# Kernel optimization log

Measured on AMD Instinct MI355X. Metric: run time of the kernel, lower is better.

## Reference

```python
import jax, jax.numpy as jnp
import numpy as np

B, N, M, C = 4, 4096, 4096, 256
IMG_W, IMG_H = 1242.0, 376.0  # KITTI-like image extents for keypoint coords


def setup_inputs() -> dict:
    key = jax.random.key(0)
    ks = jax.random.split(key, 12)
    s = 1.0 / np.sqrt(C)
    scale_uv = jnp.array([IMG_W, IMG_H], dtype=jnp.float32)
    return {
        "nodes_L": jax.random.normal(ks[0], (B, N, C), jnp.float32),
        "nodes_R": jax.random.normal(ks[1], (B, M, C), jnp.float32),
        "kpts_L": jax.random.uniform(ks[2], (B, N, 2), jnp.float32) * scale_uv,
        "kpts_R": jax.random.uniform(ks[3], (B, M, 2), jnp.float32) * scale_uv,
        "Wq": jax.random.normal(ks[4], (C, C), jnp.float32) * s,
        "bq": jnp.zeros((C,), jnp.float32),
        "Wk": jax.random.normal(ks[5], (C, C), jnp.float32) * s,
        "bk": jnp.zeros((C,), jnp.float32),
        "Wv": jax.random.normal(ks[6], (C, C), jnp.float32) * s,
        "bv": jnp.zeros((C,), jnp.float32),
        "Wm": jax.random.normal(ks[7], (C, C), jnp.float32) * s,
        "bm": jnp.zeros((C,), jnp.float32),
    }


def reference(nodes_L, nodes_R, kpts_L, kpts_R, Wq, bq, Wk, bk, Wv, bv, Wm, bm):
    dim = nodes_L.shape[-1]
    # torch.nn.Linear: y = x @ W.T + b  (W is [out, in])
    Q = jnp.einsum('bnc,dc->bnd', nodes_L, Wq) + bq  # [B,N,C]
    K = jnp.einsum('bmc,dc->bmd', nodes_R, Wk) + bk  # [B,M,C]
    V = jnp.einsum('bmc,dc->bmd', nodes_R, Wv) + bv  # [B,M,C]

    # Epipolar geometric mask from keypoint coordinates
    dist_v = jnp.abs(kpts_L[:, :, 1:2] - kpts_R[:, None, :, 1])  # [B,N,M]
    dist_u = kpts_L[:, :, 0:1] - kpts_R[:, None, :, 0]           # [B,N,M]
    mask = (dist_v < 3.0) & (dist_u > 0) & (dist_u < 192)

    attn = jnp.einsum('bnd,bmd->bnm', Q, K) / (dim ** 0.5)       # [B,N,M]
    attn = jnp.where(mask, attn, jnp.float32(-1e9))
    attn_weights = jax.nn.softmax(attn, axis=-1)                 # [B,N,M]

    matched_features = jnp.einsum('bnm,bmd->bnd', attn_weights, V)
    init_disparity = jnp.sum(attn_weights * dist_u, axis=-1, keepdims=True)  # [B,N,1]
    confidence = jnp.any(mask, axis=-1, keepdims=True).astype(jnp.float32)   # [B,N,1]
    out = jnp.einsum('bnd,cd->bnc', matched_features, Wm) + bm   # [B,N,C]
    return (out, init_disparity, confidence, attn_weights)
```

## Files before the change

### kernel.cpp

```cpp
#include <hip/hip_runtime.h>
#include <stdint.h>

#define CAP 192

typedef __attribute__((ext_vector_type(4))) float f32x4;
typedef __attribute__((ext_vector_type(8))) short bf16x8;

__device__ __forceinline__ float bf2f(ushort u) {
  return __uint_as_float(((unsigned)u) << 16);
}
__device__ __forceinline__ ushort f2bf(float f) {
  unsigned u = __float_as_uint(f);
  return (ushort)((u + 0x7fffu + ((u >> 16) & 1u)) >> 16);
}
__device__ __forceinline__ float wredsum(float v) {
#pragma unroll
  for (int o = 32; o; o >>= 1) v += __shfl_xor(v, o);
  return v;
}

__global__ __launch_bounds__(256) void cvt_kernel(const float* __restrict__ s,
                                                  ushort* __restrict__ d, int n4) {
  int i = blockIdx.x * 256 + threadIdx.x;
  if (i < n4) {
    float4 v = *(const float4*)(s + (size_t)i * 4);
    ushort4 o = { f2bf(v.x), f2bf(v.y), f2bf(v.z), f2bf(v.w) };
    *(ushort4*)(d + (size_t)i * 4) = o;
  }
}

__global__ __launch_bounds__(256) void cvt4_kernel(
    const float* __restrict__ s0, const float* __restrict__ s1,
    const float* __restrict__ s2, const float* __restrict__ s3,
    ushort* __restrict__ d0, ushort* __restrict__ d1,
    ushort* __restrict__ d2, ushort* __restrict__ d3) {
  int seg = blockIdx.x >> 6;
  int i = ((blockIdx.x & 63) * 256 + threadIdx.x) * 4;
  const float* s = (seg == 0) ? s0 : (seg == 1) ? s1 : (seg == 2) ? s2 : s3;
  ushort* d = (seg == 0) ? d0 : (seg == 1) ? d1 : (seg == 2) ? d2 : d3;
  float4 v = *(const float4*)(s + i);
  ushort4 o = { f2bf(v.x), f2bf(v.y), f2bf(v.z), f2bf(v.w) };
  *(ushort4*)(d + i) = o;
}

template <typename OutT>
__global__ __launch_bounds__(256, 2) void gemm_bt(const ushort* __restrict__ A,
                                                  const ushort* __restrict__ W,
                                                  const float* __restrict__ bias,
                                                  OutT* __restrict__ Y, int R) {
  __shared__ __align__(16) ushort As[128 * 32];
  __shared__ __align__(16) ushort Bs[128 * 32];
  int tid = threadIdx.x;
  int lane = tid & 63, wid = tid >> 6;
  int bm = blockIdx.x >> 1, bn = blockIdx.x & 1;
  int r0 = bm * 128, c0 = bn * 128;
  int wr = wid >> 1, wc = wid & 1;
  f32x4 acc[4][4] = {};
  for (int k0 = 0; k0 < 256; k0 += 32) {
    __syncthreads();
#pragma unroll
    for (int p = 0; p < 2; ++p) {
      int u = p * 2048 + tid * 8;
      int row = u >> 5, col = u & 31;
      *(bf16x8*)&As[u] = *(const bf16x8*)(A + (size_t)(r0 + row) * 256 + k0 + col);
      *(bf16x8*)&Bs[u] = *(const bf16x8*)(W + (size_t)(c0 + row) * 256 + k0 + col);
    }
    __syncthreads();
    bf16x8 af[4], bfr[4];
    int rsel = lane & 15, ksel = (lane >> 4) * 8;
#pragma unroll
    for (int m = 0; m < 4; ++m)
      af[m] = *(bf16x8*)&As[(wr * 64 + m * 16 + rsel) * 32 + ksel];
#pragma unroll
    for (int n = 0; n < 4; ++n)
      bfr[n] = *(bf16x8*)&Bs[(wc * 64 + n * 16 + rsel) * 32 + ksel];
#pragma unroll
    for (int m = 0; m < 4; ++m)
#pragma unroll
      for (int n = 0; n < 4; ++n)
        acc[m][n] = __builtin_amdgcn_mfma_f32_16x16x32_bf16(af[m], bfr[n], acc[m][n], 0, 0, 0);
  }
  int rbase = r0 + wr * 64 + ((lane >> 4) * 4);
  int cbase = c0 + wc * 64 + (lane & 15);
#pragma unroll
  for (int n = 0; n < 4; ++n) {
    float bv = bias[cbase + n * 16];
#pragma unroll
    for (int m = 0; m < 4; ++m) {
#pragma unroll
      for (int j = 0; j < 4; ++j) {
        float v = acc[m][n][j] + bv;
        size_t idx = (size_t)(rbase + m * 16 + j) * 256 + (cbase + n * 16);
        if constexpr (sizeof(OutT) == 2) Y[idx] = (OutT)f2bf(v);
        else Y[idx] = (OutT)v;
      }
    }
  }
}

__global__ __launch_bounds__(256) void batch_stats(const float* __restrict__ kptsR,
                                                   const ushort* __restrict__ Vb,
                                                   float* __restrict__ sum_uR,
                                                   float* __restrict__ sumV) {
  int b = blockIdx.x >> 4;
  int m0 = (blockIdx.x & 15) * 256;
  int c = threadIdx.x;
  float s = 0.f;
  for (int mm = 0; mm < 256; ++mm)
    s += bf2f(Vb[((size_t)(b * 4096 + m0 + mm)) * 256 + c]);
  atomicAdd(&sumV[b * 256 + c], s);
  float su = kptsR[((size_t)(b * 4096 + m0 + threadIdx.x)) * 2];
  su = wredsum(su);
  __shared__ float red[4];
  if ((threadIdx.x & 63) == 0) red[threadIdx.x >> 6] = su;
  __syncthreads();
  if (threadIdx.x == 0) atomicAdd(&sum_uR[b], red[0] + red[1] + red[2] + red[3]);
}

__global__ __launch_bounds__(512, 2) void attn_rows(
    const float* __restrict__ kptsL, const float* __restrict__ kptsR,
    const ushort* __restrict__ Qb, const ushort* __restrict__ Kb,
    const ushort* __restrict__ Vb, const float* __restrict__ sum_uR,
    const float* __restrict__ sumV, float* __restrict__ disp_out,
    float* __restrict__ conf_out, ushort* __restrict__ matched,
    int* __restrict__ rowcnt, int2* __restrict__ rowlist) {
  __shared__ float2 kR[4096];
  __shared__ int bufM[8][CAP];
  __shared__ float bufD[8][CAP];
  __shared__ float bufS[8][CAP];
  int tid = threadIdx.x, lane = tid & 63, wid = tid >> 6;
  int b = blockIdx.x >> 9;
  int n = ((blockIdx.x & 511) << 3) + wid;
  int row = (b << 12) + n;
  const float2* kRsrc = (const float2*)kptsR + (size_t)b * 4096;
  for (int i = tid; i < 4096; i += 512) kR[i] = kRsrc[i];
  __syncthreads();
  float2 kL = ((const float2*)kptsL)[(size_t)b * 4096 + n];
  ushort4 qv = *(const ushort4*)(Qb + (size_t)row * 256 + lane * 4);
  float q0 = bf2f(qv.x), q1 = bf2f(qv.y), q2 = bf2f(qv.z), q3 = bf2f(qv.w);
  int cnt = 0;
  for (int m0 = 0; m0 < 4096; m0 += 64) {
    float2 kr = kR[m0 + lane];
    float dv = fabsf(kL.y - kr.y);
    float du = kL.x - kr.x;
    bool hit = (dv < 3.0f) && (du > 0.0f) && (du < 192.0f);
    unsigned long long bal = __ballot(hit);
    while (bal) {
      int src = __ffsll((unsigned long long)bal) - 1;
      bal &= bal - 1;
      float dus = __shfl(du, src);
      if (cnt < CAP) {
        if (lane == 0) { bufM[wid][cnt] = m0 + src; bufD[wid][cnt] = dus; }
        cnt++;
      }
    }
  }
  float conf, disp;
  if (cnt == 0) {
    conf = 0.f;
    disp = kL.x - sum_uR[b] * (1.f / 4096.f);
    float v0 = sumV[b * 256 + lane * 4 + 0] * (1.f / 4096.f);
    float v1 = sumV[b * 256 + lane * 4 + 1] * (1.f / 4096.f);
    float v2 = sumV[b * 256 + lane * 4 + 2] * (1.f / 4096.f);
    float v3 = sumV[b * 256 + lane * 4 + 3] * (1.f / 4096.f);
    if (lane == 0) rowcnt[row] = 0;
    ushort4 st = { f2bf(v0), f2bf(v1), f2bf(v2), f2bf(v3) };
    *(ushort4*)(matched + (size_t)row * 256 + lane * 4) = st;
  } else {
    float mx = -1e30f;
    for (int i = 0; i < cnt; ++i) {
      int m = bufM[wid][i];
      ushort4 kv = *(const ushort4*)(Kb + ((size_t)(b * 4096 + m)) * 256 + lane * 4);
      float p = q0 * bf2f(kv.x) + q1 * bf2f(kv.y) + q2 * bf2f(kv.z) + q3 * bf2f(kv.w);
      p = wredsum(p);
      float s = p * 0.0625f;
      if (lane == 0) bufS[wid][i] = s;
      mx = fmaxf(mx, s);
    }
    float psum = 0.f, pdisp = 0.f;
    for (int i = lane; i < cnt; i += 64) {
      float e = expf(bufS[wid][i] - mx);
      bufS[wid][i] = e;
      psum += e;
      pdisp += e * bufD[wid][i];
    }
    psum = wredsum(psum);
    pdisp = wredsum(pdisp);
    float inv = 1.f / psum;
    disp = pdisp * inv;
    conf = 1.f;
    for (int i = lane; i < cnt; i += 64) {
      int2 e;
      e.x = bufM[wid][i];
      e.y = __float_as_int(bufS[wid][i] * inv);
      rowlist[(size_t)row * CAP + i] = e;
    }
    if (lane == 0) rowcnt[row] = cnt;
    float a0 = 0, a1 = 0, a2 = 0, a3 = 0;
    for (int i = 0; i < cnt; ++i) {
      float w = bufS[wid][i] * inv;
      int m = bufM[wid][i];
      ushort4 vv = *(const ushort4*)(Vb + ((size_t)(b * 4096 + m)) * 256 + lane * 4);
      a0 += w * bf2f(vv.x); a1 += w * bf2f(vv.y);
      a2 += w * bf2f(vv.z); a3 += w * bf2f(vv.w);
    }
    ushort4 st = { f2bf(a0), f2bf(a1), f2bf(a2), f2bf(a3) };
    *(ushort4*)(matched + (size_t)row * 256 + lane * 4) = st;
  }
  if (lane == 0) { disp_out[row] = disp; conf_out[row] = conf; }
}

__global__ __launch_bounds__(256) void fill_attn(const int* __restrict__ rowcnt,
                                                 const int2* __restrict__ rowlist,
                                                 float* __restrict__ attn) {
  __shared__ __align__(16) float rowbuf[4096];
  int row = blockIdx.x, tid = threadIdx.x;
  int cnt = rowcnt[row];
  float fill = (cnt == 0) ? (1.f / 4096.f) : 0.f;
  float4* rb4 = (float4*)rowbuf;
  float4 fv = make_float4(fill, fill, fill, fill);
#pragma unroll
  for (int j = 0; j < 4; ++j) rb4[j * 256 + tid] = fv;
  __syncthreads();
  for (int i = tid; i < cnt; i += 256) {
    int2 e = rowlist[(size_t)row * CAP + i];
    rowbuf[e.x] = __int_as_float(e.y);
  }
  __syncthreads();
  float4* dst = (float4*)(attn + (size_t)row * 4096);
#pragma unroll
  for (int j = 0; j < 4; ++j) dst[j * 256 + tid] = rb4[j * 256 + tid];
}

extern "C" void kernel_launch(void* const* d_in, const int* in_sizes, int n_in,
                              void* d_out, int out_size, void* d_ws, size_t ws_size,
                              hipStream_t stream) {
  const float* nodes_L = (const float*)d_in[0];
  const float* nodes_R = (const float*)d_in[1];
  const float* kpts_L = (const float*)d_in[2];
  const float* kpts_R = (const float*)d_in[3];
  const float* Wq = (const float*)d_in[4];
  const float* bq = (const float*)d_in[5];
  const float* Wk = (const float*)d_in[6];
  const float* bk = (const float*)d_in[7];
  const float* Wv = (const float*)d_in[8];
  const float* bv = (const float*)d_in[9];
  const float* Wm = (const float*)d_in[10];
  const float* bm = (const float*)d_in[11];

  float* out = (float*)d_out;
  float* disp = out + 4194304;
  float* conf = disp + 16384;
  float* attn = conf + 16384;

  char* ws = (char*)d_ws;
  ushort* Xl = (ushort*)(ws + 0);
  ushort* Xr = (ushort*)(ws + 8388608);
  ushort* Wqb = (ushort*)(ws + 16777216);
  ushort* Wkb = Wqb + 65536;
  ushort* Wvb = Wkb + 65536;
  ushort* Wmb = Wvb + 65536;
  ushort* Qb = (ushort*)(ws + 17301504);
  ushort* Kb = (ushort*)(ws + 25690112);
  ushort* Vb = (ushort*)(ws + 34078720);
  ushort* matched = (ushort*)(ws + 42467328);
  float* sum_uR = (float*)(ws + 50855936);
  float* sumV = sum_uR + 16;
  int* rowcnt = (int*)(ws + 50864128);
  int2* rowlist = (int2*)(ws + 50929664);

  hipMemsetAsync(sum_uR, 0, (16 + 1024) * 4, stream);
  cvt_kernel<<<4096, 256, 0, stream>>>(nodes_L, Xl, 1048576);
  cvt_kernel<<<4096, 256, 0, stream>>>(nodes_R, Xr, 1048576);
  cvt4_kernel<<<256, 256, 0, stream>>>(Wq, Wk, Wv, Wm, Wqb, Wkb, Wvb, Wmb);
  gemm_bt<ushort><<<256, 256, 0, stream>>>(Xl, Wqb, bq, Qb, 16384);
  gemm_bt<ushort><<<256, 256, 0, stream>>>(Xr, Wkb, bk, Kb, 16384);
  gemm_bt<ushort><<<256, 256, 0, stream>>>(Xr, Wvb, bv, Vb, 16384);
  batch_stats<<<64, 256, 0, stream>>>(kpts_R, Vb, sum_uR, sumV);
  attn_rows<<<2048, 512, 0, stream>>>(kpts_L, kpts_R, Qb, Kb, Vb, sum_uR, sumV,
                                      disp, conf, matched, rowcnt, rowlist);
  fill_attn<<<16384, 256, 0, stream>>>(rowcnt, rowlist, attn);
  gemm_bt<float><<<256, 256, 0, stream>>>(matched, Wmb, bm, out, 16384);
}
```

Measured before the change: 442.9 us.

## Fuse QKV GEMMs, compute mean V algebraically, split attn fill/scatter

Merges the three projection GEMMs into one 768-block launch. The per-batch mean of V is now computed by summing fp32 nodes_R and projecting the sum through Wv, instead of reducing the bf16 V output. Candidate collection in attn_rows uses a ballot/popcount prefix instead of a serial per-hit loop, and the K dot products and V accumulation are unrolled by two to overlap loads. The attention matrix fill becomes a nontemporal constant store followed by a separate sparse scatter kernel, replacing the LDS row-staging pass. The extra scatter launch and the write-after-write ordering between the two attn kernels are the trade-offs.

```diff
diff --git a/kernel.cpp b/kernel.cpp
--- a/kernel.cpp
+++ b/kernel.cpp
@@ -44,15 +44,14 @@
 }
 
 template <typename OutT>
-__global__ __launch_bounds__(256, 2) void gemm_bt(const ushort* __restrict__ A,
-                                                  const ushort* __restrict__ W,
-                                                  const float* __restrict__ bias,
-                                                  OutT* __restrict__ Y, int R) {
-  __shared__ __align__(16) ushort As[128 * 32];
-  __shared__ __align__(16) ushort Bs[128 * 32];
+__device__ __forceinline__ void gemm_body(const ushort* __restrict__ A,
+                                          const ushort* __restrict__ W,
+                                          const float* __restrict__ bias,
+                                          OutT* __restrict__ Y, int blk,
+                                          ushort* As, ushort* Bs) {
   int tid = threadIdx.x;
   int lane = tid & 63, wid = tid >> 6;
-  int bm = blockIdx.x >> 1, bn = blockIdx.x & 1;
+  int bm = blk >> 1, bn = blk & 1;
   int r0 = bm * 128, c0 = bn * 128;
   int wr = wid >> 1, wc = wid & 1;
   f32x4 acc[4][4] = {};
@@ -98,30 +97,85 @@
   }
 }
 
-__global__ __launch_bounds__(256) void batch_stats(const float* __restrict__ kptsR,
-                                                   const ushort* __restrict__ Vb,
-                                                   float* __restrict__ sum_uR,
-                                                   float* __restrict__ sumV) {
-  int b = blockIdx.x >> 4;
-  int m0 = (blockIdx.x & 15) * 256;
-  int c = threadIdx.x;
-  float s = 0.f;
-  for (int mm = 0; mm < 256; ++mm)
-    s += bf2f(Vb[((size_t)(b * 4096 + m0 + mm)) * 256 + c]);
-  atomicAdd(&sumV[b * 256 + c], s);
-  float su = kptsR[((size_t)(b * 4096 + m0 + threadIdx.x)) * 2];
-  su = wredsum(su);
-  __shared__ float red[4];
-  if ((threadIdx.x & 63) == 0) red[threadIdx.x >> 6] = su;
+__global__ __launch_bounds__(256, 2) void gemm3(
+    const ushort* __restrict__ Xl, const ushort* __restrict__ Xr,
+    const ushort* __restrict__ Wqb, const ushort* __restrict__ Wkb,
+    const ushort* __restrict__ Wvb, const float* __restrict__ bq,
+    const float* __restrict__ bk, const float* __restrict__ bv,
+    ushort* __restrict__ Qb, ushort* __restrict__ Kb, ushort* __restrict__ Vb) {
+  __shared__ __align__(16) ushort As[128 * 32];
+  __shared__ __align__(16) ushort Bs[128 * 32];
+  int which = blockIdx.x >> 8;
+  int blk = blockIdx.x & 255;
+  const ushort* A = (which == 0) ? Xl : Xr;
+  const ushort* W = (which == 0) ? Wqb : (which == 1) ? Wkb : Wvb;
+  const float* bias = (which == 0) ? bq : (which == 1) ? bk : bv;
+  ushort* Y = (which == 0) ? Qb : (which == 1) ? Kb : Vb;
+  gemm_body<ushort>(A, W, bias, Y, blk, As, Bs);
+}
+
+__global__ __launch_bounds__(256, 2) void gemm_out(const ushort* __restrict__ A,
+                                                   const ushort* __restrict__ W,
+                                                   const float* __restrict__ bias,
+                                                   float* __restrict__ Y) {
+  __shared__ __align__(16) ushort As[128 * 32];
+  __shared__ __align__(16) ushort Bs[128 * 32];
+  gemm_body<float>(A, W, bias, Y, blockIdx.x, As, Bs);
+}
+
+__global__ __launch_bounds__(256) void sum_nodes(const float* __restrict__ nodesR,
+                                                 const float* __restrict__ kptsR,
+                                                 float* __restrict__ S,
+                                                 float* __restrict__ sumU) {
+  int b = blockIdx.x >> 4, ch = blockIdx.x & 15;
+  int t = threadIdx.x;
+  int c4 = (t & 63) * 4;
+  int r0 = b * 4096 + ch * 256 + (t >> 6);
+  float4 acc = {0.f, 0.f, 0.f, 0.f};
+  for (int k = 0; k < 64; ++k) {
+    float4 v = *(const float4*)(nodesR + (size_t)(r0 + k * 4) * 256 + c4);
+    acc.x += v.x; acc.y += v.y; acc.z += v.z; acc.w += v.w;
+  }
+  __shared__ float4 red[256];
+  red[t] = acc;
+  float u = kptsR[(size_t)(b * 4096 + ch * 256 + t) * 2];
+  u = wredsum(u);
+  __shared__ float ured[4];
+  if ((t & 63) == 0) ured[t >> 6] = u;
   __syncthreads();
-  if (threadIdx.x == 0) atomicAdd(&sum_uR[b], red[0] + red[1] + red[2] + red[3]);
+  if (t < 64) {
+    float4 x = red[t], y = red[t + 64], z = red[t + 128], w = red[t + 192];
+    atomicAdd(&S[b * 256 + c4 + 0], x.x + y.x + z.x + w.x);
+    atomicAdd(&S[b * 256 + c4 + 1], x.y + y.y + z.y + w.y);
+    atomicAdd(&S[b * 256 + c4 + 2], x.z + y.z + z.z + w.z);
+    atomicAdd(&S[b * 256 + c4 + 3], x.w + y.w + z.w + w.w);
+  }
+  if (t == 0) atomicAdd(&sumU[b], ured[0] + ured[1] + ured[2] + ured[3]);
+}
+
+__global__ __launch_bounds__(256) void proj_mean(const float* __restrict__ S,
+                                                 const float* __restrict__ sumU,
+                                                 const float* __restrict__ Wv,
+                                                 const float* __restrict__ bv,
+                                                 ushort* __restrict__ meanVb,
+                                                 float* __restrict__ meanU) {
+  int b = blockIdx.x, c = threadIdx.x;
+  const float* s = S + b * 256;
+  float acc = 0.f;
+  for (int k = 0; k < 256; k += 4) {
+    float4 w = *(const float4*)(Wv + (size_t)c * 256 + k);
+    acc += s[k] * w.x + s[k + 1] * w.y + s[k + 2] * w.z + s[k + 3] * w.w;
+  }
+  float mv = acc * (1.f / 4096.f) + bv[c];
+  meanVb[b * 256 + c] = f2bf(mv);
+  if (c == 0) meanU[b] = sumU[b] * (1.f / 4096.f);
 }
 
 __global__ __launch_bounds__(512, 2) void attn_rows(
     const float* __restrict__ kptsL, const float* __restrict__ kptsR,
     const ushort* __restrict__ Qb, const ushort* __restrict__ Kb,
-    const ushort* __restrict__ Vb, const float* __restrict__ sum_uR,
-    const float* __restrict__ sumV, float* __restrict__ disp_out,
+    const ushort* __restrict__ Vb, const float* __restrict__ meanU,
+    const ushort* __restrict__ meanVb, float* __restrict__ disp_out,
     float* __restrict__ conf_out, ushort* __restrict__ matched,
     int* __restrict__ rowcnt, int2* __restrict__ rowlist) {
   __shared__ float2 kR[4096];
@@ -132,12 +186,14 @@
   int b = blockIdx.x >> 9;
   int n = ((blockIdx.x & 511) << 3) + wid;
   int row = (b << 12) + n;
-  const float2* kRsrc = (const float2*)kptsR + (size_t)b * 4096;
+  int bb = b << 12;
+  const float2* kRsrc = (const float2*)kptsR + (size_t)bb;
   for (int i = tid; i < 4096; i += 512) kR[i] = kRsrc[i];
   __syncthreads();
-  float2 kL = ((const float2*)kptsL)[(size_t)b * 4096 + n];
+  float2 kL = ((const float2*)kptsL)[(size_t)row];
   ushort4 qv = *(const ushort4*)(Qb + (size_t)row * 256 + lane * 4);
   float q0 = bf2f(qv.x), q1 = bf2f(qv.y), q2 = bf2f(qv.z), q3 = bf2f(qv.w);
+
   int cnt = 0;
   for (int m0 = 0; m0 < 4096; m0 += 64) {
     float2 kr = kR[m0 + lane];
@@ -145,64 +201,87 @@
     float du = kL.x - kr.x;
     bool hit = (dv < 3.0f) && (du > 0.0f) && (du < 192.0f);
     unsigned long long bal = __ballot(hit);
-    while (bal) {
-      int src = __ffsll((unsigned long long)bal) - 1;
-      bal &= bal - 1;
-      float dus = __shfl(du, src);
-      if (cnt < CAP) {
-        if (lane == 0) { bufM[wid][cnt] = m0 + src; bufD[wid][cnt] = dus; }
-        cnt++;
+    if (bal) {
+      if (hit) {
+        int pos = cnt + (int)__popcll(bal & ((1ull << lane) - 1ull));
+        if (pos < CAP) { bufM[wid][pos] = m0 + lane; bufD[wid][pos] = du; }
       }
-    }
-  }
+      cnt += (int)__popcll(bal);
+    }
+  }
+  if (cnt > CAP) cnt = CAP;
+
   float conf, disp;
   if (cnt == 0) {
     conf = 0.f;
-    disp = kL.x - sum_uR[b] * (1.f / 4096.f);
-    float v0 = sumV[b * 256 + lane * 4 + 0] * (1.f / 4096.f);
-    float v1 = sumV[b * 256 + lane * 4 + 1] * (1.f / 4096.f);
-    float v2 = sumV[b * 256 + lane * 4 + 2] * (1.f / 4096.f);
-    float v3 = sumV[b * 256 + lane * 4 + 3] * (1.f / 4096.f);
+    disp = kL.x - meanU[b];
     if (lane == 0) rowcnt[row] = 0;
-    ushort4 st = { f2bf(v0), f2bf(v1), f2bf(v2), f2bf(v3) };
+    ushort4 st = *(const ushort4*)(meanVb + b * 256 + lane * 4);
     *(ushort4*)(matched + (size_t)row * 256 + lane * 4) = st;
   } else {
     float mx = -1e30f;
-    for (int i = 0; i < cnt; ++i) {
-      int m = bufM[wid][i];
-      ushort4 kv = *(const ushort4*)(Kb + ((size_t)(b * 4096 + m)) * 256 + lane * 4);
-      float p = q0 * bf2f(kv.x) + q1 * bf2f(kv.y) + q2 * bf2f(kv.z) + q3 * bf2f(kv.w);
-      p = wredsum(p);
-      float s = p * 0.0625f;
-      if (lane == 0) bufS[wid][i] = s;
-      mx = fmaxf(mx, s);
+    int i = 0;
+    for (; i + 1 < cnt; i += 2) {
+      int ma = bufM[wid][i], mb = bufM[wid][i + 1];
+      ushort4 ka = *(const ushort4*)(Kb + ((size_t)(bb + ma)) * 256 + lane * 4);
+      ushort4 kb2 = *(const ushort4*)(Kb + ((size_t)(bb + mb)) * 256 + lane * 4);
+      float pa = q0 * bf2f(ka.x) + q1 * bf2f(ka.y) + q2 * bf2f(ka.z) + q3 * bf2f(ka.w);
+      float pb = q0 * bf2f(kb2.x) + q1 * bf2f(kb2.y) + q2 * bf2f(kb2.z) + q3 * bf2f(kb2.w);
+#pragma unroll
+      for (int o = 32; o; o >>= 1) {
+        pa += __shfl_xor(pa, o);
+        pb += __shfl_xor(pb, o);
+      }
+      float sa = pa * 0.0625f, sb = pb * 0.0625f;
+      if (lane == 0) { bufS[wid][i] = sa; bufS[wid][i + 1] = sb; }
+      mx = fmaxf(mx, fmaxf(sa, sb));
+    }
+    if (i < cnt) {
+      int ma = bufM[wid][i];
+      ushort4 ka = *(const ushort4*)(Kb + ((size_t)(bb + ma)) * 256 + lane * 4);
+      float pa = q0 * bf2f(ka.x) + q1 * bf2f(ka.y) + q2 * bf2f(ka.z) + q3 * bf2f(ka.w);
+      pa = wredsum(pa);
+      float sa = pa * 0.0625f;
+      if (lane == 0) bufS[wid][i] = sa;
+      mx = fmaxf(mx, sa);
     }
     float psum = 0.f, pdisp = 0.f;
-    for (int i = lane; i < cnt; i += 64) {
-      float e = expf(bufS[wid][i] - mx);
-      bufS[wid][i] = e;
+    for (int k = lane; k < cnt; k += 64) {
+      float e = expf(bufS[wid][k] - mx);
+      bufS[wid][k] = e;
       psum += e;
-      pdisp += e * bufD[wid][i];
+      pdisp += e * bufD[wid][k];
     }
     psum = wredsum(psum);
     pdisp = wredsum(pdisp);
     float inv = 1.f / psum;
     disp = pdisp * inv;
     conf = 1.f;
-    for (int i = lane; i < cnt; i += 64) {
+    for (int k = lane; k < cnt; k += 64) {
       int2 e;
-      e.x = bufM[wid][i];
-      e.y = __float_as_int(bufS[wid][i] * inv);
-      rowlist[(size_t)row * CAP + i] = e;
+      e.x = bufM[wid][k];
+      e.y = __float_as_int(bufS[wid][k] * inv);
+      rowlist[(size_t)row * CAP + k] = e;
     }
     if (lane == 0) rowcnt[row] = cnt;
-    float a0 = 0, a1 = 0, a2 = 0, a3 = 0;
-    for (int i = 0; i < cnt; ++i) {
-      float w = bufS[wid][i] * inv;
-      int m = bufM[wid][i];
-      ushort4 vv = *(const ushort4*)(Vb + ((size_t)(b * 4096 + m)) * 256 + lane * 4);
-      a0 += w * bf2f(vv.x); a1 += w * bf2f(vv.y);
-      a2 += w * bf2f(vv.z); a3 += w * bf2f(vv.w);
+    float a0 = 0.f, a1 = 0.f, a2 = 0.f, a3 = 0.f;
+    i = 0;
+    for (; i + 1 < cnt; i += 2) {
+      float wa = bufS[wid][i] * inv, wb = bufS[wid][i + 1] * inv;
+      int ma = bufM[wid][i], mb = bufM[wid][i + 1];
+      ushort4 va = *(const ushort4*)(Vb + ((size_t)(bb + ma)) * 256 + lane * 4);
+      ushort4 vb2 = *(const ushort4*)(Vb + ((size_t)(bb + mb)) * 256 + lane * 4);
+      a0 += wa * bf2f(va.x) + wb * bf2f(vb2.x);
+      a1 += wa * bf2f(va.y) + wb * bf2f(vb2.y);
+      a2 += wa * bf2f(va.z) + wb * bf2f(vb2.z);
+      a3 += wa * bf2f(va.w) + wb * bf2f(vb2.w);
+    }
+    if (i < cnt) {
+      float wa = bufS[wid][i] * inv;
+      int ma = bufM[wid][i];
+      ushort4 va = *(const ushort4*)(Vb + ((size_t)(bb + ma)) * 256 + lane * 4);
+      a0 += wa * bf2f(va.x); a1 += wa * bf2f(va.y);
+      a2 += wa * bf2f(va.z); a3 += wa * bf2f(va.w);
     }
     ushort4 st = { f2bf(a0), f2bf(a1), f2bf(a2), f2bf(a3) };
     *(ushort4*)(matched + (size_t)row * 256 + lane * 4) = st;
@@ -211,25 +290,31 @@
 }
 
 __global__ __launch_bounds__(256) void fill_attn(const int* __restrict__ rowcnt,
-                                                 const int2* __restrict__ rowlist,
                                                  float* __restrict__ attn) {
-  __shared__ __align__(16) float rowbuf[4096];
-  int row = blockIdx.x, tid = threadIdx.x;
+  int r0 = blockIdx.x * 8;
+  int tid = threadIdx.x;
+#pragma unroll
+  for (int r = 0; r < 8; ++r) {
+    int row = r0 + r;
+    float fill = (rowcnt[row] == 0) ? (1.f / 4096.f) : 0.f;
+    f32x4 fv = { fill, fill, fill, fill };
+    f32x4* dst = (f32x4*)(attn + (size_t)row * 4096);
+#pragma unroll
+    for (int j = 0; j < 4; ++j)
+      __builtin_nontemporal_store(fv, dst + j * 256 + tid);
+  }
+}
+
+__global__ __launch_bounds__(256) void scatter_attn(const int* __restrict__ rowcnt,
+                                                    const int2* __restrict__ rowlist,
+                                                    float* __restrict__ attn) {
+  int row = blockIdx.x * 4 + (threadIdx.x >> 6);
+  int lane = threadIdx.x & 63;
   int cnt = rowcnt[row];
-  float fill = (cnt == 0) ? (1.f / 4096.f) : 0.f;
-  float4* rb4 = (float4*)rowbuf;
-  float4 fv = make_float4(fill, fill, fill, fill);
-#pragma unroll
-  for (int j = 0; j < 4; ++j) rb4[j * 256 + tid] = fv;
-  __syncthreads();
-  for (int i = tid; i < cnt; i += 256) {
+  for (int i = lane; i < cnt; i += 64) {
     int2 e = rowlist[(size_t)row * CAP + i];
-    rowbuf[e.x] = __int_as_float(e.y);
-  }
-  __syncthreads();
-  float4* dst = (float4*)(attn + (size_t)row * 4096);
-#pragma unroll
-  for (int j = 0; j < 4; ++j) dst[j * 256 + tid] = rb4[j * 256 + tid];
+    attn[(size_t)row * 4096 + e.x] = __int_as_float(e.y);
+  }
 }
 
 extern "C" void kernel_launch(void* const* d_in, const int* in_sizes, int n_in,
@@ -264,21 +349,23 @@
   ushort* Kb = (ushort*)(ws + 25690112);
   ushort* Vb = (ushort*)(ws + 34078720);
   ushort* matched = (ushort*)(ws + 42467328);
-  float* sum_uR = (float*)(ws + 50855936);
-  float* sumV = sum_uR + 16;
+  float* S = (float*)(ws + 50855936);
+  float* sumU = (float*)(ws + 50860032);
+  float* meanU = (float*)(ws + 50860096);
+  ushort* meanVb = (ushort*)(ws + 50860160);
   int* rowcnt = (int*)(ws + 50864128);
   int2* rowlist = (int2*)(ws + 50929664);
 
-  hipMemsetAsync(sum_uR, 0, (16 + 1024) * 4, stream);
+  (void)hipMemsetAsync(S, 0, 4096 + 64, stream);
   cvt_kernel<<<4096, 256, 0, stream>>>(nodes_L, Xl, 1048576);
   cvt_kernel<<<4096, 256, 0, stream>>>(nodes_R, Xr, 1048576);
   cvt4_kernel<<<256, 256, 0, stream>>>(Wq, Wk, Wv, Wm, Wqb, Wkb, Wvb, Wmb);
-  gemm_bt<ushort><<<256, 256, 0, stream>>>(Xl, Wqb, bq, Qb, 16384);
-  gemm_bt<ushort><<<256, 256, 0, stream>>>(Xr, Wkb, bk, Kb, 16384);
-  gemm_bt<ushort><<<256, 256, 0, stream>>>(Xr, Wvb, bv, Vb, 16384);
-  batch_stats<<<64, 256, 0, stream>>>(kpts_R, Vb, sum_uR, sumV);
-  attn_rows<<<2048, 512, 0, stream>>>(kpts_L, kpts_R, Qb, Kb, Vb, sum_uR, sumV,
+  sum_nodes<<<64, 256, 0, stream>>>(nodes_R, kpts_R, S, sumU);
+  gemm3<<<768, 256, 0, stream>>>(Xl, Xr, Wqb, Wkb, Wvb, bq, bk, bv, Qb, Kb, Vb);
+  proj_mean<<<4, 256, 0, stream>>>(S, sumU, Wv, bv, meanVb, meanU);
+  attn_rows<<<2048, 512, 0, stream>>>(kpts_L, kpts_R, Qb, Kb, Vb, meanU, meanVb,
                                       disp, conf, matched, rowcnt, rowlist);
-  fill_attn<<<16384, 256, 0, stream>>>(rowcnt, rowlist, attn);
-  gemm_bt<float><<<256, 256, 0, stream>>>(matched, Wmb, bm, out, 16384);
-}
+  fill_attn<<<2048, 256, 0, stream>>>(rowcnt, attn);
+  scatter_attn<<<4096, 256, 0, stream>>>(rowcnt, rowlist, attn);
+  gemm_out<<<256, 256, 0, stream>>>(matched, Wmb, bm, out);
+}
```

Measured after the change: 460.2 us. +3.9%, slower.
